# Optimization experiments

Hardware: AMD Instinct MI355X
Metric: run time of the kernel (lower is better)

## Reference

```python
import jax, jax.numpy as jnp
import numpy as np

EPS_NORM = 1e-12
EPS_ABS = 1e-12


def _stack3(x):
    # x: [B, T, C] -> [B, T, 3, C] with left-shift, identity, right-shift taps
    prev = jnp.pad(x[:, :-1, :], ((0, 0), (1, 0), (0, 0)))
    nxt = jnp.pad(x[:, 1:, :], ((0, 0), (0, 1), (0, 0)))
    return jnp.stack([prev, x, nxt], axis=2)


def _l2_norm(x, axis):
    # matches layer's l2_normal: sqrt(max(sum(x^2), eps)), keepdims
    sq = jnp.sum(jnp.square(x), axis=axis, keepdims=True)
    return jnp.sqrt(jnp.maximum(sq, EPS_NORM))


def setup_inputs() -> dict:
    key = jax.random.key(0)
    k1, k2 = jax.random.split(key)
    B, T, C, K, U = 32, 4096, 128, 3, 256
    inputs = jax.random.normal(k1, (B, T, C), dtype=jnp.float32)
    # glorot uniform for w: limit = sqrt(6/(fan_in+fan_out)) with fan_in=C*K, fan_out=U
    limit = np.sqrt(6.0 / (C * K + U)).astype(np.float32)
    w = jax.random.uniform(k2, (1, C * K, U), dtype=jnp.float32, minval=-limit, maxval=limit)
    b = jnp.zeros((U,), dtype=jnp.float32)
    p = jnp.ones((U,), dtype=jnp.float32)
    q = jnp.zeros((1,), dtype=jnp.float32)
    return {"inputs": inputs, "w": w, "b": b, "p": p, "q": q}


def reference(inputs, w, b, p, q):
    B, T, C = inputs.shape
    U = w.shape[-1]
    x = _stack3(inputs).reshape(B, T, 3 * C)          # [B, T, 3C] (tap-major, matches tf stack+reshape)
    q2 = jnp.square(q)                                 # [1]
    x_norm = _l2_norm(x, axis=2) + q2                  # [B, T, 1]
    w_norm = _l2_norm(w, axis=1) + q2                  # [1, 1, U]
    w2 = w[0]                                          # [3C, U]
    sign = jnp.sign(jnp.einsum('btk,ku->btu', x, w2))  # sign of raw matmul
    y = jnp.einsum('btk,ku->btu', x / x_norm, w2 / w_norm[0])
    y = jnp.abs(y) + EPS_ABS
    y = jnp.power(y, jnp.square(p))                    # broadcast over units
    y = sign * y + b
    return y
```

## Files before the change

kernel.cpp:

```cpp
#include <hip/hip_runtime.h>

typedef __attribute__((ext_vector_type(8))) short short8;
typedef __attribute__((ext_vector_type(4))) float f32x4;

#define T_DIM 4096
#define C_DIM 128
#define U_DIM 256
#define BM 128
#define NROWS 130
#define LDK 136

__device__ __forceinline__ unsigned short f2bf(float f) {
    unsigned int u = __float_as_uint(f);
    u += 0x7FFFu + ((u >> 16) & 1u);
    return (unsigned short)(u >> 16);
}

__global__ void prep_kernel(const float* __restrict__ w,
                            const float* __restrict__ b,
                            const float* __restrict__ p,
                            const float* __restrict__ q,
                            unsigned short* __restrict__ wfrag,
                            float* __restrict__ winv,
                            float* __restrict__ p2,
                            float* __restrict__ bc) {
    if (blockIdx.x < 48) {
        int idx = blockIdx.x * 256 + threadIdx.x;
        int l  = idx & 63;
        int nt = (idx >> 6) & 15;
        int ks = idx >> 10;
        int n  = nt * 16 + (l & 15);
        int k0 = ks * 32 + ((l >> 4) << 3);
        #pragma unroll
        for (int j = 0; j < 8; ++j) {
            wfrag[(size_t)idx * 8 + j] = f2bf(w[(k0 + j) * U_DIM + n]);
        }
    } else {
        int u = threadIdx.x;
        float ss = 0.f;
        for (int k = 0; k < 3 * C_DIM; ++k) {
            float v = w[k * U_DIM + u];
            ss += v * v;
        }
        float q2 = q[0] * q[0];
        winv[u] = 1.0f / (sqrtf(fmaxf(ss, 1e-12f)) + q2);
        float pv = p[u];
        p2[u] = pv * pv;
        bc[u] = b[u];
    }
}

__global__ __launch_bounds__(512, 4) void cossim_main(
        const float* __restrict__ inp,
        const unsigned short* __restrict__ wfrag,
        const float* __restrict__ winv,
        const float* __restrict__ p2g,
        const float* __restrict__ bg,
        const float* __restrict__ qg,
        float* __restrict__ out) {
    __shared__ unsigned short inp_s[NROWS][LDK];
    __shared__ float ss_s[NROWS];
    __shared__ float xninv_s[BM];

    const int tid  = threadIdx.x;
    const int bidx = blockIdx.x;
    const int bb   = bidx >> 5;
    const int t0   = (bidx & 31) * BM;

    {
        const int r0 = tid >> 5;
        const int lc = (tid & 31) * 4;
        for (int r = r0; r < NROWS; r += 16) {
            int t = t0 + r - 1;
            float4 v = make_float4(0.f, 0.f, 0.f, 0.f);
            if (t >= 0 && t < T_DIM) {
                v = *(const float4*)(inp + ((size_t)bb * T_DIM + t) * C_DIM + lc);
            }
            float part = v.x * v.x + v.y * v.y + v.z * v.z + v.w * v.w;
            #pragma unroll
            for (int o = 16; o > 0; o >>= 1) part += __shfl_xor(part, o, 32);
            if ((tid & 31) == 0) ss_s[r] = part;
            ushort4 sv;
            sv.x = f2bf(v.x); sv.y = f2bf(v.y); sv.z = f2bf(v.z); sv.w = f2bf(v.w);
            *(ushort4*)(&inp_s[r][lc]) = sv;
        }
    }
    __syncthreads();
    if (tid < BM) {
        float s3 = ss_s[tid] + ss_s[tid + 1] + ss_s[tid + 2];
        float q2 = qg[0] * qg[0];
        xninv_s[tid] = 1.0f / (sqrtf(fmaxf(s3, 1e-12f)) + q2);
    }
    __syncthreads();

    const int wid = tid >> 6;
    const int l   = tid & 63;
    const int tw  = wid >> 2;
    const int uw  = wid & 3;
    const int l15 = l & 15;
    const int lg  = l >> 4;

    f32x4 acc[4][4];
    #pragma unroll
    for (int tf = 0; tf < 4; ++tf)
        #pragma unroll
        for (int uf = 0; uf < 4; ++uf)
            acc[tf][uf] = (f32x4){0.f, 0.f, 0.f, 0.f};

    const short8* wf = (const short8*)wfrag;

    for (int ks = 0; ks < 12; ++ks) {
        const int tap = ks >> 2;
        const int c0  = (ks & 3) * 32 + lg * 8;
        short8 xv[4], wv[4];
        #pragma unroll
        for (int tf = 0; tf < 4; ++tf) {
            int row = tw * 64 + tf * 16 + l15 + tap;
            xv[tf] = *(const short8*)(&inp_s[row][c0]);
        }
        #pragma unroll
        for (int uf = 0; uf < 4; ++uf) {
            wv[uf] = wf[(size_t)(ks * 16 + uw * 4 + uf) * 64 + l];
        }
        #pragma unroll
        for (int tf = 0; tf < 4; ++tf)
            #pragma unroll
            for (int uf = 0; uf < 4; ++uf)
                acc[tf][uf] = __builtin_amdgcn_mfma_f32_16x16x32_bf16(
                    wv[uf], xv[tf], acc[tf][uf], 0, 0, 0);
    }

    #pragma unroll
    for (int tf = 0; tf < 4; ++tf) {
        int trow = tw * 64 + tf * 16 + l15;
        float xi = xninv_s[trow];
        float* orow = out + ((size_t)bb * T_DIM + t0 + trow) * U_DIM;
        #pragma unroll
        for (int uf = 0; uf < 4; ++uf) {
            int uc = uw * 64 + uf * 16 + lg * 4;
            f32x4 wiv = *(const f32x4*)(winv + uc);
            f32x4 ppv = *(const f32x4*)(p2g + uc);
            f32x4 bbv = *(const f32x4*)(bg + uc);
            f32x4 r;
            #pragma unroll
            for (int j = 0; j < 4; ++j) {
                float raw = acc[tf][uf][j];
                float y   = raw * xi * wiv[j];
                float ay  = fabsf(y) + 1e-12f;
                float pw  = ppv[j];
                float rr  = (pw == 1.0f) ? ay : powf(ay, pw);
                float s   = (raw > 0.f) ? 1.f : ((raw < 0.f) ? -1.f : 0.f);
                r[j] = s * rr + bbv[j];
            }
            *(f32x4*)(orow + uc) = r;
        }
    }
}

extern "C" void kernel_launch(void* const* d_in, const int* in_sizes, int n_in,
                              void* d_out, int out_size, void* d_ws, size_t ws_size,
                              hipStream_t stream) {
    const float* inp = (const float*)d_in[0];
    const float* w   = (const float*)d_in[1];
    const float* b   = (const float*)d_in[2];
    const float* p   = (const float*)d_in[3];
    const float* q   = (const float*)d_in[4];
    float* out = (float*)d_out;

    unsigned short* wfrag = (unsigned short*)d_ws;
    float* winv = (float*)((char*)d_ws + 196608);
    float* p2   = winv + 256;
    float* bc   = p2 + 256;

    prep_kernel<<<49, 256, 0, stream>>>(w, b, p, q, wfrag, winv, p2, bc);
    cossim_main<<<1024, 512, 0, stream>>>(inp, wfrag, winv, p2, bc, q, out);
}
```

Before: 75.82 us.

## Pre-convert input to swizzled bf16 buffer and stream it via global_load_lds

Adds a prep pass that converts the whole input to a zero-padded, XOR-swizzled bf16 global buffer and precomputes per-row inverse norms. The main kernel then uses smaller 64-row tiles with 256 threads and copies the bf16 tile directly into LDS with global_load_lds, avoiding in-kernel conversion and LDS bank conflicts. This removes the halo-load and norm work from the GEMM kernel but adds an extra full write and read of a bf16 copy of the input (about 32 MB) plus a large prep launch.

```diff
diff --git a/kernel.cpp b/kernel.cpp
--- a/kernel.cpp
+++ b/kernel.cpp
@@ -6,9 +6,9 @@
 #define T_DIM 4096
 #define C_DIM 128
 #define U_DIM 256
-#define BM 128
-#define NROWS 130
-#define LDK 136
+#define BM 64
+#define NR 68
+#define TP2 4098
 
 __device__ __forceinline__ unsigned short f2bf(float f) {
     unsigned int u = __float_as_uint(f);
@@ -16,89 +16,109 @@
     return (unsigned short)(u >> 16);
 }
 
-__global__ void prep_kernel(const float* __restrict__ w,
-                            const float* __restrict__ b,
-                            const float* __restrict__ p,
-                            const float* __restrict__ q,
-                            unsigned short* __restrict__ wfrag,
-                            float* __restrict__ winv,
-                            float* __restrict__ p2,
-                            float* __restrict__ bc) {
-    if (blockIdx.x < 48) {
-        int idx = blockIdx.x * 256 + threadIdx.x;
-        int l  = idx & 63;
-        int nt = (idx >> 6) & 15;
-        int ks = idx >> 10;
-        int n  = nt * 16 + (l & 15);
-        int k0 = ks * 32 + ((l >> 4) << 3);
-        #pragma unroll
-        for (int j = 0; j < 8; ++j) {
-            wfrag[(size_t)idx * 8 + j] = f2bf(w[(k0 + j) * U_DIM + n]);
+__global__ __launch_bounds__(320) void prep_all(
+        const float* __restrict__ inp, const float* __restrict__ w,
+        const float* __restrict__ b, const float* __restrict__ p,
+        const float* __restrict__ q,
+        unsigned short* __restrict__ xbf, unsigned short* __restrict__ wfrag,
+        float* __restrict__ xninv, float* __restrict__ winv,
+        float* __restrict__ p2, float* __restrict__ bc) {
+    const int blk = blockIdx.x;
+    const int tid = threadIdx.x;
+    if (blk < 16384) {
+        __shared__ float ss_s[10];
+        const int bb    = blk >> 9;
+        const int tbase = (blk & 511) * 8;
+        const int gidx  = tid >> 5;
+        const int hl    = tid & 31;
+        const int t     = tbase - 1 + gidx;
+        float4 v = make_float4(0.f, 0.f, 0.f, 0.f);
+        if ((unsigned)t < T_DIM)
+            v = *(const float4*)(inp + ((size_t)bb * T_DIM + t) * C_DIM + hl * 4);
+        float part = v.x * v.x + v.y * v.y + v.z * v.z + v.w * v.w;
+        #pragma unroll
+        for (int o = 16; o > 0; o >>= 1) part += __shfl_xor(part, o, 32);
+        if (hl == 0) ss_s[gidx] = part;
+        if ((unsigned)t < T_DIM) {
+            int c  = hl >> 1;
+            int cs = c ^ ((t + 1) & 7);
+            ushort4 sv;
+            sv.x = f2bf(v.x); sv.y = f2bf(v.y); sv.z = f2bf(v.z); sv.w = f2bf(v.w);
+            *(ushort4*)(xbf + ((size_t)bb * TP2 + t + 1) * 128 + cs * 8 + (hl & 1) * 4) = sv;
+        }
+        if (tbase == 0 && tid < 32) {
+            ushort4 z = make_ushort4(0, 0, 0, 0);
+            ((ushort4*)(xbf + (size_t)bb * TP2 * 128))[tid] = z;
+        }
+        if (tbase == T_DIM - 8 && tid < 32) {
+            ushort4 z = make_ushort4(0, 0, 0, 0);
+            ((ushort4*)(xbf + ((size_t)bb * TP2 + T_DIM + 1) * 128))[tid] = z;
+        }
+        __syncthreads();
+        if (tid < 8) {
+            float q2v = q[0] * q[0];
+            float s3  = ss_s[tid] + ss_s[tid + 1] + ss_s[tid + 2];
+            xninv[(size_t)bb * T_DIM + tbase + tid] =
+                1.0f / (sqrtf(fmaxf(s3, 1e-12f)) + q2v);
+        }
+    } else if (blk < 16432) {
+        if (tid < 256) {
+            int idx = (blk - 16384) * 256 + tid;
+            int ll = idx & 63;
+            int nt = (idx >> 6) & 15;
+            int ks = idx >> 10;
+            int n  = nt * 16 + (ll & 15);
+            int k0 = ks * 32 + ((ll >> 4) << 3);
+            #pragma unroll
+            for (int j = 0; j < 8; ++j)
+                wfrag[(size_t)idx * 8 + j] = f2bf(w[(k0 + j) * U_DIM + n]);
         }
     } else {
-        int u = threadIdx.x;
-        float ss = 0.f;
-        for (int k = 0; k < 3 * C_DIM; ++k) {
-            float v = w[k * U_DIM + u];
-            ss += v * v;
-        }
-        float q2 = q[0] * q[0];
-        winv[u] = 1.0f / (sqrtf(fmaxf(ss, 1e-12f)) + q2);
-        float pv = p[u];
-        p2[u] = pv * pv;
-        bc[u] = b[u];
-    }
-}
-
-__global__ __launch_bounds__(512, 4) void cossim_main(
-        const float* __restrict__ inp,
+        if (tid < 256) {
+            int u = tid;
+            float ss = 0.f;
+            for (int k = 0; k < 3 * C_DIM; ++k) {
+                float v = w[k * U_DIM + u];
+                ss += v * v;
+            }
+            float q2v = q[0] * q[0];
+            winv[u] = 1.0f / (sqrtf(fmaxf(ss, 1e-12f)) + q2v);
+            float pv = p[u];
+            p2[u] = pv * pv;
+            bc[u] = b[u];
+        }
+    }
+}
+
+__global__ __launch_bounds__(256, 4) void cossim_main(
+        const unsigned short* __restrict__ xbf,
         const unsigned short* __restrict__ wfrag,
+        const float* __restrict__ xninv,
         const float* __restrict__ winv,
         const float* __restrict__ p2g,
         const float* __restrict__ bg,
-        const float* __restrict__ qg,
         float* __restrict__ out) {
-    __shared__ unsigned short inp_s[NROWS][LDK];
-    __shared__ float ss_s[NROWS];
-    __shared__ float xninv_s[BM];
-
-    const int tid  = threadIdx.x;
-    const int bidx = blockIdx.x;
-    const int bb   = bidx >> 5;
-    const int t0   = (bidx & 31) * BM;
-
-    {
-        const int r0 = tid >> 5;
-        const int lc = (tid & 31) * 4;
-        for (int r = r0; r < NROWS; r += 16) {
-            int t = t0 + r - 1;
-            float4 v = make_float4(0.f, 0.f, 0.f, 0.f);
-            if (t >= 0 && t < T_DIM) {
-                v = *(const float4*)(inp + ((size_t)bb * T_DIM + t) * C_DIM + lc);
-            }
-            float part = v.x * v.x + v.y * v.y + v.z * v.z + v.w * v.w;
-            #pragma unroll
-            for (int o = 16; o > 0; o >>= 1) part += __shfl_xor(part, o, 32);
-            if ((tid & 31) == 0) ss_s[r] = part;
-            ushort4 sv;
-            sv.x = f2bf(v.x); sv.y = f2bf(v.y); sv.z = f2bf(v.z); sv.w = f2bf(v.w);
-            *(ushort4*)(&inp_s[r][lc]) = sv;
-        }
-    }
-    __syncthreads();
-    if (tid < BM) {
-        float s3 = ss_s[tid] + ss_s[tid + 1] + ss_s[tid + 2];
-        float q2 = qg[0] * qg[0];
-        xninv_s[tid] = 1.0f / (sqrtf(fmaxf(s3, 1e-12f)) + q2);
-    }
-    __syncthreads();
-
+    __shared__ unsigned short xs[NR * 128];
+
+    const int tid = threadIdx.x;
+    const int bb  = blockIdx.x >> 6;
+    const int t0  = (blockIdx.x & 63) * BM;
     const int wid = tid >> 6;
     const int l   = tid & 63;
-    const int tw  = wid >> 2;
-    const int uw  = wid & 3;
     const int l15 = l & 15;
     const int lg  = l >> 4;
+
+    {
+        const unsigned short* src = xbf + ((size_t)bb * TP2 + t0) * 128;
+        for (int j = wid; j < 17; j += 4) {
+            const unsigned short* gp = src + j * 512 + l * 8;
+            __builtin_amdgcn_global_load_lds(
+                (const __attribute__((address_space(1))) unsigned int*)gp,
+                (__attribute__((address_space(3))) unsigned int*)(xs + j * 512),
+                16, 0, 0);
+        }
+    }
+    __syncthreads();
 
     f32x4 acc[4][4];
     #pragma unroll
@@ -109,35 +129,36 @@
 
     const short8* wf = (const short8*)wfrag;
 
+    #pragma unroll
     for (int ks = 0; ks < 12; ++ks) {
         const int tap = ks >> 2;
-        const int c0  = (ks & 3) * 32 + lg * 8;
-        short8 xv[4], wv[4];
+        const int cb  = (ks & 3) * 4;
+        short8 xv[4], wvv[4];
         #pragma unroll
         for (int tf = 0; tf < 4; ++tf) {
-            int row = tw * 64 + tf * 16 + l15 + tap;
-            xv[tf] = *(const short8*)(&inp_s[row][c0]);
-        }
-        #pragma unroll
-        for (int uf = 0; uf < 4; ++uf) {
-            wv[uf] = wf[(size_t)(ks * 16 + uw * 4 + uf) * 64 + l];
-        }
+            int r  = tf * 16 + l15 + tap;
+            int ch = (cb + lg) ^ (r & 7);
+            xv[tf] = *(const short8*)(xs + r * 128 + ch * 8);
+        }
+        #pragma unroll
+        for (int uf = 0; uf < 4; ++uf)
+            wvv[uf] = wf[(size_t)(ks * 16 + wid * 4 + uf) * 64 + l];
         #pragma unroll
         for (int tf = 0; tf < 4; ++tf)
             #pragma unroll
             for (int uf = 0; uf < 4; ++uf)
                 acc[tf][uf] = __builtin_amdgcn_mfma_f32_16x16x32_bf16(
-                    wv[uf], xv[tf], acc[tf][uf], 0, 0, 0);
+                    wvv[uf], xv[tf], acc[tf][uf], 0, 0, 0);
     }
 
     #pragma unroll
     for (int tf = 0; tf < 4; ++tf) {
-        int trow = tw * 64 + tf * 16 + l15;
-        float xi = xninv_s[trow];
-        float* orow = out + ((size_t)bb * T_DIM + t0 + trow) * U_DIM;
+        int trow = t0 + tf * 16 + l15;
+        float xi = xninv[(size_t)bb * T_DIM + trow];
+        float* orow = out + ((size_t)bb * T_DIM + trow) * U_DIM;
         #pragma unroll
         for (int uf = 0; uf < 4; ++uf) {
-            int uc = uw * 64 + uf * 16 + lg * 4;
+            int uc = wid * 64 + uf * 16 + lg * 4;
             f32x4 wiv = *(const f32x4*)(winv + uc);
             f32x4 ppv = *(const f32x4*)(p2g + uc);
             f32x4 bbv = *(const f32x4*)(bg + uc);
@@ -148,7 +169,8 @@
                 float y   = raw * xi * wiv[j];
                 float ay  = fabsf(y) + 1e-12f;
                 float pw  = ppv[j];
-                float rr  = (pw == 1.0f) ? ay : powf(ay, pw);
+                float rr  = ay;
+                if (pw != 1.0f) rr = powf(ay, pw);
                 float s   = (raw > 0.f) ? 1.f : ((raw < 0.f) ? -1.f : 0.f);
                 r[j] = s * rr + bbv[j];
             }
@@ -167,11 +189,13 @@
     const float* q   = (const float*)d_in[4];
     float* out = (float*)d_out;
 
-    unsigned short* wfrag = (unsigned short*)d_ws;
-    float* winv = (float*)((char*)d_ws + 196608);
-    float* p2   = winv + 256;
-    float* bc   = p2 + 256;
-
-    prep_kernel<<<49, 256, 0, stream>>>(w, b, p, q, wfrag, winv, p2, bc);
-    cossim_main<<<1024, 512, 0, stream>>>(inp, wfrag, winv, p2, bc, q, out);
-}
+    unsigned short* xbf   = (unsigned short*)d_ws;
+    unsigned short* wfrag = (unsigned short*)((char*)d_ws + 33570816);
+    float* xninv = (float*)((char*)d_ws + 33570816 + 196608);
+    float* winv  = xninv + 32 * 4096;
+    float* p2    = winv + 256;
+    float* bc    = p2 + 256;
+
+    prep_all<<<16433, 320, 0, stream>>>(inp, w, b, p, q, xbf, wfrag, xninv, winv, p2, bc);
+    cossim_main<<<2048, 256, 0, stream>>>(xbf, wfrag, xninv, winv, p2, bc, out);
+}
```

Result: slower. 87.29 us (+15.1%).

## Make main kernel persistent with register-resident weights and prefetched input tiles

Applied to the files above, without the earlier changes.

Each block now loops over 8 consecutive 64-row time tiles for one half of the output units. It keeps its slice of the bf16 weight fragments in registers for the whole loop and prefetches the next input tile into registers while the current tile's MFMAs run. The grid shrinks to 512 blocks of 256 threads, and the block index is remapped so neighbouring blocks spread across batches. Per-row norm handling and the pow/sign epilogue are simplified to use exp2/log2 and copysign. The aim is to cut repeated global weight loads and hide input-load latency, at the cost of higher register pressure, lower parallelism, and each input tile being loaded by two blocks.

```diff
diff --git a/kernel.cpp b/kernel.cpp
--- a/kernel.cpp
+++ b/kernel.cpp
@@ -6,9 +6,10 @@
 #define T_DIM 4096
 #define C_DIM 128
 #define U_DIM 256
-#define BM 128
-#define NROWS 130
+#define BM 64
+#define NROWS 66
 #define LDK 136
+#define NT 8
 
 __device__ __forceinline__ unsigned short f2bf(float f) {
     unsigned int u = __float_as_uint(f);
@@ -50,7 +51,41 @@
     }
 }
 
-__global__ __launch_bounds__(512, 4) void cossim_main(
+#define STAGE_LOAD(t0v, vv)                                                    \
+    do {                                                                       \
+        _Pragma("unroll")                                                      \
+        for (int i_ = 0; i_ < 9; ++i_) {                                       \
+            int r_ = r0 + i_ * 8;                                              \
+            int t_ = (t0v) + r_ - 1;                                           \
+            float4 val_ = make_float4(0.f, 0.f, 0.f, 0.f);                     \
+            if (r_ < NROWS && (unsigned)t_ < T_DIM)                            \
+                val_ = *(const float4*)(inp + ((size_t)bb * T_DIM + t_) * C_DIM + lc); \
+            vv[i_] = val_;                                                     \
+        }                                                                      \
+    } while (0)
+
+#define STAGE_WRITE(vv)                                                        \
+    do {                                                                       \
+        _Pragma("unroll")                                                      \
+        for (int i_ = 0; i_ < 9; ++i_) {                                       \
+            int r_ = r0 + i_ * 8;                                              \
+            if (r_ < NROWS) {                                                  \
+                float4 val_ = vv[i_];                                          \
+                float part_ = val_.x * val_.x + val_.y * val_.y                \
+                            + val_.z * val_.z + val_.w * val_.w;               \
+                _Pragma("unroll")                                              \
+                for (int o_ = 16; o_ > 0; o_ >>= 1)                            \
+                    part_ += __shfl_xor(part_, o_, 32);                        \
+                if ((tid & 31) == 0) ss_s[r_] = part_;                         \
+                ushort4 sv_;                                                   \
+                sv_.x = f2bf(val_.x); sv_.y = f2bf(val_.y);                    \
+                sv_.z = f2bf(val_.z); sv_.w = f2bf(val_.w);                    \
+                *(ushort4*)(&inp_s[r_][lc]) = sv_;                             \
+            }                                                                  \
+        }                                                                      \
+    } while (0)
+
+__global__ __launch_bounds__(256, 2) void cossim_main(
         const float* __restrict__ inp,
         const unsigned short* __restrict__ wfrag,
         const float* __restrict__ winv,
@@ -60,99 +95,104 @@
         float* __restrict__ out) {
     __shared__ unsigned short inp_s[NROWS][LDK];
     __shared__ float ss_s[NROWS];
-    __shared__ float xninv_s[BM];
-
-    const int tid  = threadIdx.x;
-    const int bidx = blockIdx.x;
-    const int bb   = bidx >> 5;
-    const int t0   = (bidx & 31) * BM;
-
-    {
-        const int r0 = tid >> 5;
-        const int lc = (tid & 31) * 4;
-        for (int r = r0; r < NROWS; r += 16) {
-            int t = t0 + r - 1;
-            float4 v = make_float4(0.f, 0.f, 0.f, 0.f);
-            if (t >= 0 && t < T_DIM) {
-                v = *(const float4*)(inp + ((size_t)bb * T_DIM + t) * C_DIM + lc);
-            }
-            float part = v.x * v.x + v.y * v.y + v.z * v.z + v.w * v.w;
-            #pragma unroll
-            for (int o = 16; o > 0; o >>= 1) part += __shfl_xor(part, o, 32);
-            if ((tid & 31) == 0) ss_s[r] = part;
-            ushort4 sv;
-            sv.x = f2bf(v.x); sv.y = f2bf(v.y); sv.z = f2bf(v.z); sv.w = f2bf(v.w);
-            *(ushort4*)(&inp_s[r][lc]) = sv;
-        }
-    }
-    __syncthreads();
-    if (tid < BM) {
-        float s3 = ss_s[tid] + ss_s[tid + 1] + ss_s[tid + 2];
-        float q2 = qg[0] * qg[0];
-        xninv_s[tid] = 1.0f / (sqrtf(fmaxf(s3, 1e-12f)) + q2);
-    }
-    __syncthreads();
+
+    const int tid = threadIdx.x;
+    int bid = blockIdx.x;
+    bid = (bid & 7) * 64 + (bid >> 3);
+    const int bb = bid >> 4;
+    const int tg = (bid >> 1) & 7;
+    const int uh = bid & 1;
 
     const int wid = tid >> 6;
     const int l   = tid & 63;
-    const int tw  = wid >> 2;
-    const int uw  = wid & 3;
     const int l15 = l & 15;
     const int lg  = l >> 4;
-
-    f32x4 acc[4][4];
+    const int r0  = tid >> 5;
+    const int lc  = (tid & 31) * 4;
+
+    const float q2 = qg[0] * qg[0];
+    const short8* wf = (const short8*)wfrag;
+
+    short8 wr[12][2];
     #pragma unroll
-    for (int tf = 0; tf < 4; ++tf)
-        #pragma unroll
-        for (int uf = 0; uf < 4; ++uf)
-            acc[tf][uf] = (f32x4){0.f, 0.f, 0.f, 0.f};
-
-    const short8* wf = (const short8*)wfrag;
-
-    for (int ks = 0; ks < 12; ++ks) {
-        const int tap = ks >> 2;
-        const int c0  = (ks & 3) * 32 + lg * 8;
-        short8 xv[4], wv[4];
+    for (int ks = 0; ks < 12; ++ks)
+        #pragma unroll
+        for (int uf = 0; uf < 2; ++uf)
+            wr[ks][uf] = wf[(size_t)(ks * 16 + uh * 8 + wid * 2 + uf) * 64 + l];
+
+    const int ucb = uh * 128 + wid * 32;
+    f32x4 wiv[2], ppv[2], bbv[2];
+    #pragma unroll
+    for (int uf = 0; uf < 2; ++uf) {
+        int uc = ucb + uf * 16 + lg * 4;
+        wiv[uf] = *(const f32x4*)(winv + uc);
+        ppv[uf] = *(const f32x4*)(p2g + uc);
+        bbv[uf] = *(const f32x4*)(bg + uc);
+    }
+
+    const int tbase = tg * (NT * BM);
+    {
+        float4 v0[9];
+        STAGE_LOAD(tbase, v0);
+        STAGE_WRITE(v0);
+    }
+    __syncthreads();
+
+    for (int it = 0; it < NT; ++it) {
+        const int t0 = tbase + it * BM;
+
+        float4 vn[9];
+        if (it + 1 < NT) STAGE_LOAD(t0 + BM, vn);
+
+        f32x4 acc[4][2];
+        #pragma unroll
+        for (int tf = 0; tf < 4; ++tf)
+            #pragma unroll
+            for (int uf = 0; uf < 2; ++uf)
+                acc[tf][uf] = (f32x4){0.f, 0.f, 0.f, 0.f};
+
+        #pragma unroll
+        for (int ks = 0; ks < 12; ++ks) {
+            const int tap = ks >> 2;
+            const int c0  = (ks & 3) * 32 + lg * 8;
+            short8 xv[4];
+            #pragma unroll
+            for (int tf = 0; tf < 4; ++tf)
+                xv[tf] = *(const short8*)(&inp_s[tf * 16 + l15 + tap][c0]);
+            #pragma unroll
+            for (int tf = 0; tf < 4; ++tf)
+                #pragma unroll
+                for (int uf = 0; uf < 2; ++uf)
+                    acc[tf][uf] = __builtin_amdgcn_mfma_f32_16x16x32_bf16(
+                        wr[ks][uf], xv[tf], acc[tf][uf], 0, 0, 0);
+        }
+
         #pragma unroll
         for (int tf = 0; tf < 4; ++tf) {
-            int row = tw * 64 + tf * 16 + l15 + tap;
-            xv[tf] = *(const short8*)(&inp_s[row][c0]);
-        }
-        #pragma unroll
-        for (int uf = 0; uf < 4; ++uf) {
-            wv[uf] = wf[(size_t)(ks * 16 + uw * 4 + uf) * 64 + l];
-        }
-        #pragma unroll
-        for (int tf = 0; tf < 4; ++tf)
-            #pragma unroll
-            for (int uf = 0; uf < 4; ++uf)
-                acc[tf][uf] = __builtin_amdgcn_mfma_f32_16x16x32_bf16(
-                    wv[uf], xv[tf], acc[tf][uf], 0, 0, 0);
-    }
-
-    #pragma unroll
-    for (int tf = 0; tf < 4; ++tf) {
-        int trow = tw * 64 + tf * 16 + l15;
-        float xi = xninv_s[trow];
-        float* orow = out + ((size_t)bb * T_DIM + t0 + trow) * U_DIM;
-        #pragma unroll
-        for (int uf = 0; uf < 4; ++uf) {
-            int uc = uw * 64 + uf * 16 + lg * 4;
-            f32x4 wiv = *(const f32x4*)(winv + uc);
-            f32x4 ppv = *(const f32x4*)(p2g + uc);
-            f32x4 bbv = *(const f32x4*)(bg + uc);
-            f32x4 r;
-            #pragma unroll
-            for (int j = 0; j < 4; ++j) {
-                float raw = acc[tf][uf][j];
-                float y   = raw * xi * wiv[j];
-                float ay  = fabsf(y) + 1e-12f;
-                float pw  = ppv[j];
-                float rr  = (pw == 1.0f) ? ay : powf(ay, pw);
-                float s   = (raw > 0.f) ? 1.f : ((raw < 0.f) ? -1.f : 0.f);
-                r[j] = s * rr + bbv[j];
+            int trow = tf * 16 + l15;
+            float s3 = ss_s[trow] + ss_s[trow + 1] + ss_s[trow + 2];
+            float xi = 1.0f / (sqrtf(fmaxf(s3, 1e-12f)) + q2);
+            float* orow = out + ((size_t)bb * T_DIM + t0 + trow) * U_DIM;
+            #pragma unroll
+            for (int uf = 0; uf < 2; ++uf) {
+                f32x4 r;
+                #pragma unroll
+                for (int j = 0; j < 4; ++j) {
+                    float raw = acc[tf][uf][j];
+                    float y   = raw * xi * wiv[uf][j];
+                    float ay  = fabsf(y) + 1e-12f;
+                    float pw  = ppv[uf][j];
+                    float rr  = (pw == 1.0f) ? ay : exp2f(pw * __log2f(ay));
+                    r[j] = __builtin_copysignf(rr, raw) + bbv[uf][j];
+                }
+                *(f32x4*)(orow + ucb + uf * 16 + lg * 4) = r;
             }
-            *(f32x4*)(orow + uc) = r;
+        }
+
+        if (it + 1 < NT) {
+            __syncthreads();
+            STAGE_WRITE(vn);
+            __syncthreads();
         }
     }
 }
@@ -173,5 +213,5 @@
     float* bc   = p2 + 256;
 
     prep_kernel<<<49, 256, 0, stream>>>(w, b, p, q, wfrag, winv, p2, bc);
-    cossim_main<<<1024, 512, 0, stream>>>(inp, wfrag, winv, p2, bc, q, out);
-}
+    cossim_main<<<512, 256, 0, stream>>>(inp, wfrag, winv, p2, bc, q, out);
+}
```

Result: faster. 66.80 us (-11.9%).
